# Kernel optimization log

Hardware: AMD Instinct MI355X
Metric: run time of the kernel (lower is better)

## Reference

```python
import jax, jax.numpy as jnp
import numpy as np

N_NODES = 20000
N_EDGES = 100000   # undirected input edges; make_directed doubles them
FEAT = 128
N_RBF = 20
NUM_CONV = 3
CUTOFF = 20.0
BOX = 10.0


def setup_inputs() -> dict:
    key = jax.random.key(0)
    ks = jax.random.split(key, 6)
    cg_xyz = jax.random.uniform(ks[0], (N_NODES, 3), jnp.float32) * BOX
    # random edges with no self-loops (avoid d=0 singularity in rbf/unit)
    src = jax.random.randint(ks[1], (N_EDGES,), 0, N_NODES)
    off = jax.random.randint(ks[2], (N_EDGES,), 1, N_NODES)
    CG_nbr_list = jnp.stack([src, (src + off) % N_NODES], axis=1)
    cg_s = jax.random.normal(ks[3], (N_NODES, FEAT), jnp.float32)

    def w(k, shape, fan_in):
        return (jax.random.normal(k, shape, jnp.float32) / np.float32(np.sqrt(fan_in)))
    kk = jax.random.split(ks[4], 7)
    params = dict(
        msg_W1=w(kk[0], (NUM_CONV, FEAT, FEAT), FEAT),
        msg_b1=jnp.zeros((NUM_CONV, FEAT), jnp.float32),
        msg_W2=w(kk[1], (NUM_CONV, 3 * FEAT, FEAT), FEAT),
        msg_b2=jnp.zeros((NUM_CONV, 3 * FEAT), jnp.float32),
        dist_W=w(kk[2], (NUM_CONV, 3 * FEAT, N_RBF), N_RBF),
        dist_b=jnp.zeros((NUM_CONV, 3 * FEAT), jnp.float32),
        upd_U=w(kk[3], (NUM_CONV, FEAT, FEAT), FEAT),
        upd_V=w(kk[4], (NUM_CONV, FEAT, FEAT), FEAT),
        upd_sW1=w(kk[5], (NUM_CONV, FEAT, 2 * FEAT), 2 * FEAT),
        upd_sb1=jnp.zeros((NUM_CONV, FEAT), jnp.float32),
        upd_sW2=w(kk[6], (NUM_CONV, 3 * FEAT, FEAT), FEAT),
        upd_sb2=jnp.zeros((NUM_CONV, 3 * FEAT), jnp.float32),
    )
    return dict(cg_xyz=cg_xyz, CG_nbr_list=CG_nbr_list, cg_s=cg_s, **params)


def _forward(cg_xyz, cg_s, nbr, msg_W1, msg_b1, msg_W2, msg_b2, dist_W, dist_b,
             upd_U, upd_V, upd_sW1, upd_sb1, upd_sW2, upd_sb2):
    N = cg_s.shape[0]
    # make_directed: input is undirected -> append flipped edges
    nbrs = jnp.concatenate([nbr, nbr[:, ::-1]], axis=0)   # [E, 2]
    i, j = nbrs[:, 0], nbrs[:, 1]
    r_ij = cg_xyz[j] - cg_xyz[i]                           # [E, 3]
    d = jnp.linalg.norm(r_ij, axis=-1)                     # [E]
    unit = r_ij / d[:, None]
    # PainnRadialBasis: sin(k*pi*d/cutoff)/d, k=1..n_rbf
    kvec = jnp.arange(1, N_RBF + 1, dtype=cg_xyz.dtype)
    rbf = jnp.sin(kvec * jnp.pi * d[:, None] / CUTOFF) / d[:, None]   # [E, n_rbf]
    # cosine envelope
    env = jnp.where(d < CUTOFF, 0.5 * (jnp.cos(jnp.pi * d / CUTOFF) + 1.0), 0.0)

    s = cg_s
    v = jnp.zeros((N, FEAT, 3), cg_s.dtype)
    for l in range(NUM_CONV):
        # ---- MessageBlock ----
        phi = jax.nn.silu(s @ msg_W1[l].T + msg_b1[l]) @ msg_W2[l].T + msg_b2[l]  # [N, 3F]
        w_s = (rbf @ dist_W[l].T + dist_b[l]) * env[:, None]                      # [E, 3F]
        inv = (phi[j] * w_s).reshape(-1, 3, FEAT)                                 # [E, 3, F]
        dv_ij = inv[:, 2, :, None] * unit[:, None, :] + inv[:, 0, :, None] * v[j] # [E, F, 3]
        s = s + jax.ops.segment_sum(inv[:, 1, :], i, num_segments=N)
        v = v + jax.ops.segment_sum(dv_ij, i, num_segments=N)
        # ---- UpdateBlock ----
        u_v = jnp.einsum('nfd,gf->ngd', v, upd_U[l])   # [N, F, 3]
        v_v = jnp.einsum('nfd,gf->ngd', v, upd_V[l])
        v_v_norm = jnp.linalg.norm(v_v, axis=-1)       # [N, F]
        a = (jax.nn.silu(jnp.concatenate([s, v_v_norm], -1) @ upd_sW1[l].T + upd_sb1[l])
             @ upd_sW2[l].T + upd_sb2[l]).reshape(-1, 3, FEAT)  # a_vv, a_sv, a_ss
        s = s + (u_v * v_v).sum(-1) * a[:, 1, :] + a[:, 2, :]
        v = v + u_v * a[:, 0, :, None]
    return s, v


def reference(cg_xyz, CG_nbr_list, cg_s, msg_W1, msg_b1, msg_W2, msg_b2, dist_W,
              dist_b, upd_U, upd_V, upd_sW1, upd_sb1, upd_sW2, upd_sb2):
    return _forward(cg_xyz, cg_s, CG_nbr_list, msg_W1, msg_b1, msg_W2, msg_b2,
                    dist_W, dist_b, upd_U, upd_V, upd_sW1, upd_sb1, upd_sW2, upd_sb2)
```

## Files before the change

### kernel.cpp

```cpp
#include <hip/hip_runtime.h>
#include <math.h>

#define FEAT 128
#define NRBF 20
#define NCONV 3
#define PI_F 3.14159265358979323846f

typedef __attribute__((ext_vector_type(8))) short short8;
typedef __attribute__((ext_vector_type(4))) float floatx4;
typedef unsigned short ushort_t;

__device__ inline float b2f(unsigned short u) {
    union { unsigned int i; float f; } c; c.i = ((unsigned int)u) << 16; return c.f;
}
__device__ inline unsigned short f2b(float x) {
    union { float f; unsigned int i; } c; c.f = x;
    unsigned int u = c.i;
    return (unsigned short)((u + 0x7fffu + ((u >> 16) & 1u)) >> 16);
}

template<int FUSED>
__global__ __launch_bounds__(256, 2) void mlp_fused_kernel(
    const float* __restrict__ s, const float* __restrict__ vv,
    const ushort_t* __restrict__ W1h, const ushort_t* __restrict__ W1l,
    const float* __restrict__ b1,
    const ushort_t* __restrict__ W2h, const ushort_t* __restrict__ W2l,
    const float* __restrict__ b2,
    ushort_t* __restrict__ out_b,
    const float* __restrict__ uv,
    float* s_out, float* vbuf,
    float* outv,
    int M, int K1, int SP)
{
    __shared__ __align__(16) ushort_t Ah[64 * 40];
    __shared__ __align__(16) ushort_t Al[64 * 40];
    __shared__ __align__(16) ushort_t Wh[128 * 40];
    __shared__ __align__(16) ushort_t Wl[128 * 40];
    __shared__ __align__(16) ushort_t Hh[64 * 136];
    __shared__ __align__(16) ushort_t Hl[64 * 136];

    const int t    = threadIdx.x;
    const int m0   = blockIdx.x * 64;
    const int wv   = t >> 6;
    const int lane = t & 63;
    const int wn   = wv * 32;
    const int lr   = lane & 15;
    const int lk   = (lane >> 4) * 8;
    const int quad = lane >> 4;
    const int arow = t >> 3;
    const int acol = (t & 7) * 4;
    const int wrow = t >> 2;
    const int wcol = (t & 3) * 8;

    floatx4 acc[4][2] = {};

    for (int k0 = 0; k0 < K1; k0 += 32) {
        #pragma unroll
        for (int h = 0; h < 2; ++h) {
            int r = arow + h * 32;
            int m = m0 + r; if (m >= M) m = M - 1;
            float xs[4];
            if (k0 < 128) {
                float4 av = *(const float4*)(s + (long)m * 128 + k0 + acol);
                xs[0] = av.x; xs[1] = av.y; xs[2] = av.z; xs[3] = av.w;
            } else {
                long base = (long)m * 128 + (k0 - 128 + acol);
                float4 a0 = *(const float4*)(vv + base);
                float4 a1 = *(const float4*)(vv + (long)SP + base);
                float4 a2 = *(const float4*)(vv + 2 * (long)SP + base);
                xs[0] = sqrtf(a0.x * a0.x + a1.x * a1.x + a2.x * a2.x);
                xs[1] = sqrtf(a0.y * a0.y + a1.y * a1.y + a2.y * a2.y);
                xs[2] = sqrtf(a0.z * a0.z + a1.z * a1.z + a2.z * a2.z);
                xs[3] = sqrtf(a0.w * a0.w + a1.w * a1.w + a2.w * a2.w);
            }
            unsigned short hh[4], ll[4];
            #pragma unroll
            for (int q = 0; q < 4; ++q) {
                hh[q] = f2b(xs[q]);
                ll[q] = f2b(xs[q] - b2f(hh[q]));
            }
            *(ushort4*)(&Ah[r * 40 + acol]) = make_ushort4(hh[0], hh[1], hh[2], hh[3]);
            *(ushort4*)(&Al[r * 40 + acol]) = make_ushort4(ll[0], ll[1], ll[2], ll[3]);
        }
        #pragma unroll
        for (int h = 0; h < 2; ++h) {
            int r = wrow + h * 64;
            *(uint4*)(&Wh[r * 40 + wcol]) =
                *(const uint4*)(W1h + (long)r * K1 + k0 + wcol);
            *(uint4*)(&Wl[r * 40 + wcol]) =
                *(const uint4*)(W1l + (long)r * K1 + k0 + wcol);
        }
        __syncthreads();
        short8 af[4], alf[4], wf[2], wlf[2];
        #pragma unroll
        for (int i = 0; i < 4; ++i) {
            af[i]  = *(const short8*)(&Ah[(i * 16 + lr) * 40 + lk]);
            alf[i] = *(const short8*)(&Al[(i * 16 + lr) * 40 + lk]);
        }
        #pragma unroll
        for (int j = 0; j < 2; ++j) {
            wf[j]  = *(const short8*)(&Wh[(wn + j * 16 + lr) * 40 + lk]);
            wlf[j] = *(const short8*)(&Wl[(wn + j * 16 + lr) * 40 + lk]);
        }
        #pragma unroll
        for (int i = 0; i < 4; ++i)
            #pragma unroll
            for (int j = 0; j < 2; ++j) {
                acc[i][j] = __builtin_amdgcn_mfma_f32_16x16x32_bf16(
                    af[i], wf[j], acc[i][j], 0, 0, 0);
                acc[i][j] = __builtin_amdgcn_mfma_f32_16x16x32_bf16(
                    af[i], wlf[j], acc[i][j], 0, 0, 0);
                acc[i][j] = __builtin_amdgcn_mfma_f32_16x16x32_bf16(
                    alf[i], wf[j], acc[i][j], 0, 0, 0);
            }
        __syncthreads();
    }

    #pragma unroll
    for (int i = 0; i < 4; ++i)
        #pragma unroll
        for (int r = 0; r < 4; ++r) {
            int mrow = i * 16 + quad * 4 + r;
            #pragma unroll
            for (int j = 0; j < 2; ++j) {
                int kcol = wn + j * 16 + lr;
                float x = acc[i][j][r] + b1[kcol];
                x *= 1.f / (1.f + __expf(-x));
                unsigned short hh = f2b(x);
                Hh[mrow * 136 + kcol] = hh;
                Hl[mrow * 136 + kcol] = f2b(x - b2f(hh));
            }
        }

    floatx4 accS[3][4][2];
    #pragma unroll
    for (int nt = 0; nt < 3; ++nt) {
        floatx4 a2c[4][2] = {};
        for (int k0 = 0; k0 < 128; k0 += 32) {
            __syncthreads();
            #pragma unroll
            for (int h = 0; h < 2; ++h) {
                int r = wrow + h * 64;
                long wo = (long)(nt * 128 + r) * 128;
                *(uint4*)(&Wh[r * 40 + wcol]) = *(const uint4*)(W2h + wo + k0 + wcol);
                *(uint4*)(&Wl[r * 40 + wcol]) = *(const uint4*)(W2l + wo + k0 + wcol);
            }
            __syncthreads();
            short8 af[4], alf[4], wf[2], wlf[2];
            #pragma unroll
            for (int i = 0; i < 4; ++i) {
                af[i]  = *(const short8*)(&Hh[(i * 16 + lr) * 136 + k0 + lk]);
                alf[i] = *(const short8*)(&Hl[(i * 16 + lr) * 136 + k0 + lk]);
            }
            #pragma unroll
            for (int j = 0; j < 2; ++j) {
                wf[j]  = *(const short8*)(&Wh[(wn + j * 16 + lr) * 40 + lk]);
                wlf[j] = *(const short8*)(&Wl[(wn + j * 16 + lr) * 40 + lk]);
            }
            #pragma unroll
            for (int i = 0; i < 4; ++i)
                #pragma unroll
                for (int j = 0; j < 2; ++j) {
                    a2c[i][j] = __builtin_amdgcn_mfma_f32_16x16x32_bf16(
                        af[i], wf[j], a2c[i][j], 0, 0, 0);
                    a2c[i][j] = __builtin_amdgcn_mfma_f32_16x16x32_bf16(
                        af[i], wlf[j], a2c[i][j], 0, 0, 0);
                    a2c[i][j] = __builtin_amdgcn_mfma_f32_16x16x32_bf16(
                        alf[i], wf[j], a2c[i][j], 0, 0, 0);
                }
        }
        if (FUSED) {
            #pragma unroll
            for (int i = 0; i < 4; ++i)
                #pragma unroll
                for (int j = 0; j < 2; ++j)
                    accS[nt][i][j] = a2c[i][j];
        } else {
            #pragma unroll
            for (int i = 0; i < 4; ++i)
                #pragma unroll
                for (int r = 0; r < 4; ++r) {
                    int m = m0 + i * 16 + quad * 4 + r;
                    if (m >= M) continue;
                    #pragma unroll
                    for (int j = 0; j < 2; ++j) {
                        int n = nt * 128 + wn + j * 16 + lr;
                        out_b[(long)m * 384 + n] = f2b(a2c[i][j][r] + b2[n]);
                    }
                }
        }
    }

    if (FUSED) {
        #pragma unroll
        for (int i = 0; i < 4; ++i)
            #pragma unroll
            for (int r = 0; r < 4; ++r) {
                int m = m0 + i * 16 + quad * 4 + r;
                if (m >= M) continue;
                #pragma unroll
                for (int j = 0; j < 2; ++j) {
                    int g = wn + j * 16 + lr;
                    long idx = (long)m * 128 + g;
                    float a0 = accS[0][i][j][r] + b2[g];
                    float a1 = accS[1][i][j][r] + b2[128 + g];
                    float a2 = accS[2][i][j][r] + b2[256 + g];
                    float u0 = uv[idx], u1 = uv[SP + idx], u2 = uv[2 * SP + idx];
                    float w0 = vv[idx], w1 = vv[SP + idx], w2 = vv[2 * SP + idx];
                    float dot = u0 * w0 + u1 * w1 + u2 * w2;
                    s_out[idx] = s[idx] + dot * a1 + a2;
                    float x0 = vbuf[idx]          + u0 * a0;
                    float x1 = vbuf[SP + idx]     + u1 * a0;
                    float x2 = vbuf[2 * SP + idx] + u2 * a0;
                    if (outv) {
                        outv[idx * 3 + 0] = x0;
                        outv[idx * 3 + 1] = x1;
                        outv[idx * 3 + 2] = x2;
                    } else {
                        vbuf[idx]          = x0;
                        vbuf[SP + idx]     = x1;
                        vbuf[2 * SP + idx] = x2;
                    }
                }
            }
    }
}

__global__ __launch_bounds__(256) void gemm_ps_kernel(
    const ushort_t* __restrict__ Ahg, const ushort_t* __restrict__ Alg,
    const ushort_t* __restrict__ Whi, const ushort_t* __restrict__ Wlo,
    const ushort_t* __restrict__ W2h, const ushort_t* __restrict__ W2l,
    float* __restrict__ C0, float* __restrict__ C1,
    int M, int K)
{
    __shared__ __align__(16) ushort_t Ah[128 * 40];
    __shared__ __align__(16) ushort_t Al[128 * 40];
    __shared__ __align__(16) ushort_t Wh[128 * 40];
    __shared__ __align__(16) ushort_t Wl[128 * 40];
    const int t    = threadIdx.x;
    const int m0   = blockIdx.x * 128;
    const int nt   = blockIdx.y;
    const int wv   = t >> 6;
    const int lane = t & 63;
    const int wm   = (wv >> 1) * 64;
    const int wn   = (wv & 1) * 64;
    const int lr   = lane & 15;
    const int lk   = (lane >> 4) * 8;
    const int srow = t >> 2;
    const int scol = (t & 3) * 8;
    const ushort_t* Wsh = nt ? W2h : Whi;
    const ushort_t* Wsl = nt ? W2l : Wlo;

    floatx4 acc[4][4] = {};

    for (int k0 = 0; k0 < K; k0 += 32) {
        #pragma unroll
        for (int h = 0; h < 2; ++h) {
            int r = srow + h * 64;
            int m = m0 + r; if (m >= M) m = M - 1;
            *(uint4*)(&Ah[r * 40 + scol]) =
                *(const uint4*)(Ahg + (long)m * K + k0 + scol);
            *(uint4*)(&Al[r * 40 + scol]) =
                *(const uint4*)(Alg + (long)m * K + k0 + scol);
            *(uint4*)(&Wh[r * 40 + scol]) =
                *(const uint4*)(Wsh + (long)r * K + k0 + scol);
            *(uint4*)(&Wl[r * 40 + scol]) =
                *(const uint4*)(Wsl + (long)r * K + k0 + scol);
        }
        __syncthreads();
        short8 ah[4], al[4], wh[4], wl[4];
        #pragma unroll
        for (int i = 0; i < 4; ++i) {
            ah[i] = *(const short8*)(&Ah[(wm + i * 16 + lr) * 40 + lk]);
            al[i] = *(const short8*)(&Al[(wm + i * 16 + lr) * 40 + lk]);
            wh[i] = *(const short8*)(&Wh[(wn + i * 16 + lr) * 40 + lk]);
            wl[i] = *(const short8*)(&Wl[(wn + i * 16 + lr) * 40 + lk]);
        }
        #pragma unroll
        for (int i = 0; i < 4; ++i)
            #pragma unroll
            for (int j = 0; j < 4; ++j) {
                acc[i][j] = __builtin_amdgcn_mfma_f32_16x16x32_bf16(
                    ah[i], wh[j], acc[i][j], 0, 0, 0);
                acc[i][j] = __builtin_amdgcn_mfma_f32_16x16x32_bf16(
                    ah[i], wl[j], acc[i][j], 0, 0, 0);
                acc[i][j] = __builtin_amdgcn_mfma_f32_16x16x32_bf16(
                    al[i], wh[j], acc[i][j], 0, 0, 0);
            }
        __syncthreads();
    }

    float* C = nt ? C1 : C0;
    #pragma unroll
    for (int i = 0; i < 4; ++i)
        #pragma unroll
        for (int r = 0; r < 4; ++r) {
            int m = m0 + wm + i * 16 + (lane >> 4) * 4 + r;
            if (m >= M) continue;
            #pragma unroll
            for (int j = 0; j < 4; ++j) {
                int n = wn + j * 16 + lr;
                C[(long)m * 128 + n] = acc[i][j][r];
            }
        }
}

__global__ __launch_bounds__(256) void split_kernel(
    const float* __restrict__ src, ushort_t* __restrict__ hi,
    ushort_t* __restrict__ lo, int n)
{
    int i = blockIdx.x * blockDim.x + threadIdx.x;
    if (i >= n) return;
    float x = src[i];
    unsigned short h = f2b(x);
    hi[i] = h;
    lo[i] = f2b(x - b2f(h));
}

__global__ __launch_bounds__(256) void hist_kernel(
    const int* __restrict__ nbr, int* __restrict__ deg, int Ed)
{
    int e = blockIdx.x * blockDim.x + threadIdx.x;
    if (e >= Ed) return;
    int E = Ed >> 1;
    int i = (e < E) ? nbr[2 * e] : nbr[2 * (e - E) + 1];
    atomicAdd(&deg[i], 1);
}

__device__ inline int wave_incl_scan(int x, int lane)
{
    #pragma unroll
    for (int s = 1; s < 64; s <<= 1) {
        int y = __shfl_up(x, s, 64);
        if (lane >= s) x += y;
    }
    return x;
}

__global__ __launch_bounds__(1024) void scan_kernel(
    const int* __restrict__ deg, int* __restrict__ off,
    int* __restrict__ cursor, int N)
{
    __shared__ int wsum[16];
    __shared__ int carry_s;
    const int t = threadIdx.x;
    const int lane = t & 63;
    const int w = t >> 6;
    if (t == 0) { carry_s = 0; off[0] = 0; }
    __syncthreads();
    for (int base = 0; base < N; base += 1024) {
        int i = base + t;
        int x = (i < N) ? deg[i] : 0;
        int sc = wave_incl_scan(x, lane);
        if (lane == 63) wsum[w] = sc;
        __syncthreads();
        if (w == 0) {
            int v = (lane < 16) ? wsum[lane] : 0;
            int vs = wave_incl_scan(v, lane);
            if (lane < 16) wsum[lane] = vs;
        }
        __syncthreads();
        int waveoff = (w > 0) ? wsum[w - 1] : 0;
        int inc = sc + waveoff + carry_s;
        if (i < N) { off[i + 1] = inc; cursor[i] = inc - x; }
        __syncthreads();
        if (t == 1023) carry_s = inc;
        __syncthreads();
    }
}

__global__ __launch_bounds__(256) void scatter_geom_kernel(
    const int* __restrict__ nbr, const float* __restrict__ xyz,
    int* __restrict__ cursor, int* __restrict__ csr_j,
    float* __restrict__ csr_env, float* __restrict__ csr_unit,
    float* __restrict__ csr_rbfe, int Ed)
{
    int e = blockIdx.x * blockDim.x + threadIdx.x;
    if (e >= Ed) return;
    int E = Ed >> 1;
    int i, j;
    if (e < E) { i = nbr[2 * e];         j = nbr[2 * e + 1]; }
    else       { int u = e - E; i = nbr[2 * u + 1]; j = nbr[2 * u]; }

    int p = atomicAdd(&cursor[i], 1);
    csr_j[p] = j;

    float rx = xyz[3 * j + 0] - xyz[3 * i + 0];
    float ry = xyz[3 * j + 1] - xyz[3 * i + 1];
    float rz = xyz[3 * j + 2] - xyz[3 * i + 2];
    float d   = sqrtf(rx * rx + ry * ry + rz * rz);
    float inv = 1.f / d;
    csr_unit[3 * p + 0] = rx * inv;
    csr_unit[3 * p + 1] = ry * inv;
    csr_unit[3 * p + 2] = rz * inv;
    float ev = (d < 20.f) ? 0.5f * (__cosf(PI_F * d / 20.f) + 1.f) : 0.f;
    csr_env[p] = ev;
    float base = PI_F * d / 20.f;
    #pragma unroll
    for (int k = 0; k < NRBF; ++k)
        csr_rbfe[(long)p * NRBF + k] = ev * __sinf((float)(k + 1) * base) * inv;
}

__global__ __launch_bounds__(128) void edge_aggr_kernel(
    const int* __restrict__ off, const int* __restrict__ csr_j,
    const float* __restrict__ csr_env, const float* __restrict__ csr_unit,
    const float* __restrict__ csr_rbfe,
    const ushort_t* __restrict__ phib, const float* __restrict__ vold,
    const float* __restrict__ distW, const float* __restrict__ distb,
    float* __restrict__ s, float* __restrict__ vnew,
    ushort_t* __restrict__ vnh, ushort_t* __restrict__ vnl, int N, int SP)
{
    const int f = threadIdx.x;
    float w0c[NRBF], w1c[NRBF], w2c[NRBF];
    const float b0 = distb[f];
    const float b1 = distb[128 + f];
    const float b2 = distb[256 + f];
    #pragma unroll
    for (int k = 0; k < NRBF; ++k) {
        w0c[k] = distW[(long)f * NRBF + k];
        w1c[k] = distW[(long)(128 + f) * NRBF + k];
        w2c[k] = distW[(long)(256 + f) * NRBF + k];
    }

    for (int node = blockIdx.x; node < N; node += gridDim.x) {
        const int p0 = off[node], p1 = off[node + 1];
        float ssum = 0.f, v0 = 0.f, v1 = 0.f, v2 = 0.f;
        for (int p = p0; p < p1; ++p) {
            int j = csr_j[p];
            float ev = csr_env[p];
            float ux = csr_unit[3 * p + 0];
            float uy = csr_unit[3 * p + 1];
            float uz = csr_unit[3 * p + 2];
            const float* rb = csr_rbfe + (long)p * NRBF;
            float w0 = ev * b0, w1 = ev * b1, w2 = ev * b2;
            #pragma unroll
            for (int k = 0; k < NRBF; ++k) {
                float r = rb[k];
                w0 += r * w0c[k];
                w1 += r * w1c[k];
                w2 += r * w2c[k];
            }
            long jb = (long)j * 384;
            float i0 = b2f(phib[jb + f])       * w0;
            float i1 = b2f(phib[jb + 128 + f]) * w1;
            float i2 = b2f(phib[jb + 256 + f]) * w2;
            long jv = (long)j * FEAT + f;
            ssum += i1;
            v0 += i2 * ux + i0 * vold[jv];
            v1 += i2 * uy + i0 * vold[SP + jv];
            v2 += i2 * uz + i0 * vold[2 * SP + jv];
        }
        long iv = (long)node * FEAT + f;
        s[iv] += ssum;
        float n0 = vold[iv]          + v0;
        float n1 = vold[SP + iv]     + v1;
        float n2 = vold[2 * SP + iv] + v2;
        vnew[iv]          = n0;
        vnew[SP + iv]     = n1;
        vnew[2 * SP + iv] = n2;
        unsigned short h0 = f2b(n0), h1 = f2b(n1), h2 = f2b(n2);
        vnh[iv]          = h0;  vnl[iv]          = f2b(n0 - b2f(h0));
        vnh[SP + iv]     = h1;  vnl[SP + iv]     = f2b(n1 - b2f(h1));
        vnh[2 * SP + iv] = h2;  vnl[2 * SP + iv] = f2b(n2 - b2f(h2));
    }
}

__global__ __launch_bounds__(256) void init_s_kernel(
    const float* __restrict__ cg_s, float* __restrict__ s,
    float* __restrict__ vA, int nS, int nV)
{
    int idx = blockIdx.x * blockDim.x + threadIdx.x;
    if (idx < nS) s[idx] = cg_s[idx];
    if (idx < nV) vA[idx] = 0.f;
}

extern "C" void kernel_launch(void* const* d_in, const int* in_sizes, int n_in,
                              void* d_out, int out_size, void* d_ws, size_t ws_size,
                              hipStream_t stream)
{
    const float* xyz     = (const float*)d_in[0];
    const int*   nbr     = (const int*)  d_in[1];
    const float* cg_s    = (const float*)d_in[2];
    const float* msg_W1  = (const float*)d_in[3];
    const float* msg_b1  = (const float*)d_in[4];
    const float* msg_W2  = (const float*)d_in[5];
    const float* msg_b2  = (const float*)d_in[6];
    const float* dist_W  = (const float*)d_in[7];
    const float* dist_b  = (const float*)d_in[8];
    const float* upd_U   = (const float*)d_in[9];
    const float* upd_V   = (const float*)d_in[10];
    const float* upd_sW1 = (const float*)d_in[11];
    const float* upd_sb1 = (const float*)d_in[12];
    const float* upd_sW2 = (const float*)d_in[13];
    const float* upd_sb2 = (const float*)d_in[14];

    const int E  = in_sizes[1] / 2;
    const int Ed = 2 * E;
    const int N  = in_sizes[2] / FEAT;
    const int SP = N * FEAT;

    float* s    = (float*)d_out;
    float* outv = (float*)d_out + (long)SP;

    float* w = (float*)d_ws;
    size_t off_ = 0;
    auto alloc = [&](size_t nelem) {
        float* p = w + off_;
        off_ += (nelem + 255) & ~(size_t)255;
        return p;
    };
    auto allocb = [&](size_t nelem) {
        return (ushort_t*)alloc((nelem + 1) / 2);
    };
    int*   deg      = (int*)alloc((size_t)N);
    int*   off      = (int*)alloc((size_t)N + 1);
    int*   cursor   = (int*)alloc((size_t)N);
    int*   csr_j    = (int*)alloc((size_t)Ed);
    float* csr_env  = alloc((size_t)Ed);
    float* csr_unit = alloc((size_t)Ed * 3);
    float* csr_rbfe = alloc((size_t)Ed * NRBF);
    float* u_v      = alloc((size_t)3 * SP);
    float* v_v      = alloc((size_t)3 * SP);
    float* vA       = alloc((size_t)3 * SP);
    float* vB       = alloc((size_t)3 * SP);
    ushort_t* phi_b = allocb((size_t)N * 384);
    ushort_t* vnh   = allocb((size_t)3 * SP);
    ushort_t* vnl   = allocb((size_t)3 * SP);
    const int n1 = NCONV * FEAT * FEAT;
    const int n2 = NCONV * 3 * FEAT * FEAT;
    const int n3 = NCONV * FEAT * 2 * FEAT;
    ushort_t* w1h  = allocb((size_t)n1);
    ushort_t* w1l  = allocb((size_t)n1);
    ushort_t* w2h  = allocb((size_t)n2);
    ushort_t* w2l  = allocb((size_t)n2);
    ushort_t* uh   = allocb((size_t)n1);
    ushort_t* ul   = allocb((size_t)n1);
    ushort_t* vh   = allocb((size_t)n1);
    ushort_t* vl   = allocb((size_t)n1);
    ushort_t* sw1h = allocb((size_t)n3);
    ushort_t* sw1l = allocb((size_t)n3);
    ushort_t* sw2h = allocb((size_t)n2);
    ushort_t* sw2l = allocb((size_t)n2);
    (void)ws_size; (void)n_in; (void)out_size;

    split_kernel<<<(n1 + 255) / 256, 256, 0, stream>>>(msg_W1, w1h, w1l, n1);
    split_kernel<<<(n2 + 255) / 256, 256, 0, stream>>>(msg_W2, w2h, w2l, n2);
    split_kernel<<<(n1 + 255) / 256, 256, 0, stream>>>(upd_U, uh, ul, n1);
    split_kernel<<<(n1 + 255) / 256, 256, 0, stream>>>(upd_V, vh, vl, n1);
    split_kernel<<<(n3 + 255) / 256, 256, 0, stream>>>(upd_sW1, sw1h, sw1l, n3);
    split_kernel<<<(n2 + 255) / 256, 256, 0, stream>>>(upd_sW2, sw2h, sw2l, n2);

    {
        int n = 3 * SP;
        init_s_kernel<<<(n + 255) / 256, 256, 0, stream>>>(cg_s, s, vA, SP, n);
    }

    hipMemsetAsync(deg, 0, (size_t)N * sizeof(int), stream);
    hist_kernel<<<(Ed + 255) / 256, 256, 0, stream>>>(nbr, deg, Ed);
    scan_kernel<<<1, 1024, 0, stream>>>(deg, off, cursor, N);
    scatter_geom_kernel<<<(Ed + 255) / 256, 256, 0, stream>>>(
        nbr, xyz, cursor, csr_j, csr_env, csr_unit, csr_rbfe, Ed);

    float* vold = vA;
    float* vnew = vB;
    dim3 gM((N + 63) / 64, 1);
    dim3 gUV((3 * N + 127) / 128, 2);
    int edgeGrid = 2048;
    if (edgeGrid > N) edgeGrid = N;

    for (int l = 0; l < NCONV; ++l) {
        const float* b1  = msg_b1  + (long)l * FEAT;
        const float* b2  = msg_b2  + (long)l * 3 * FEAT;
        const float* dW  = dist_W  + (long)l * 3 * FEAT * NRBF;
        const float* db  = dist_b  + (long)l * 3 * FEAT;
        const float* sb1 = upd_sb1 + (long)l * FEAT;
        const float* sb2 = upd_sb2 + (long)l * 3 * FEAT;
        const long o1 = (long)l * FEAT * FEAT;
        const long o2 = (long)l * 3 * FEAT * FEAT;
        const long o3 = (long)l * FEAT * 2 * FEAT;

        mlp_fused_kernel<0><<<gM, 256, 0, stream>>>(
            s, nullptr, w1h + o1, w1l + o1, b1, w2h + o2, w2l + o2, b2,
            phi_b, nullptr, nullptr, nullptr, nullptr, N, FEAT, SP);

        edge_aggr_kernel<<<edgeGrid, 128, 0, stream>>>(
            off, csr_j, csr_env, csr_unit, csr_rbfe, phi_b, vold,
            dW, db, s, vnew, vnh, vnl, N, SP);

        gemm_ps_kernel<<<gUV, 256, 0, stream>>>(
            vnh, vnl, uh + o1, ul + o1, vh + o1, vl + o1,
            u_v, v_v, 3 * N, FEAT);

        float* ov = (l == NCONV - 1) ? outv : nullptr;
        mlp_fused_kernel<1><<<gM, 256, 0, stream>>>(
            s, v_v, sw1h + o3, sw1l + o3, sb1, sw2h + o2, sw2l + o2, sb2,
            nullptr, u_v, s, vnew, ov, N, 2 * FEAT, SP);

        float* tmp = vold; vold = vnew; vnew = tmp;
    }
}
```

Before: 768.8 us.

## Fuse next layer's message MLP into update MLP kernel epilogue

Adds a MODE 2 variant of the MLP kernel that, after the update block, writes the new s tile into shared memory as a split bf16 hi/lo pair. It then runs the next layer's message MLP (W1, SiLU, W2) on that tile, so layers 1 and 2 no longer need a separate message MLP launch or a re-read of s from global memory. It also doubles the edge aggregation grid size. The trade is more shared-memory reuse, extra barriers and register pressure in the fused kernel against one fewer launch and less memory traffic per layer.

```diff
diff --git a/kernel.cpp b/kernel.cpp
--- a/kernel.cpp
+++ b/kernel.cpp
@@ -19,7 +19,7 @@
     return (unsigned short)((u + 0x7fffu + ((u >> 16) & 1u)) >> 16);
 }
 
-template<int FUSED>
+template<int MODE>
 __global__ __launch_bounds__(256, 2) void mlp_fused_kernel(
     const float* __restrict__ s, const float* __restrict__ vv,
     const ushort_t* __restrict__ W1h, const ushort_t* __restrict__ W1l,
@@ -30,6 +30,11 @@
     const float* __restrict__ uv,
     float* s_out, float* vbuf,
     float* outv,
+    const ushort_t* __restrict__ pW1h, const ushort_t* __restrict__ pW1l,
+    const float* __restrict__ pb1,
+    const ushort_t* __restrict__ pW2h, const ushort_t* __restrict__ pW2l,
+    const float* __restrict__ pb2,
+    ushort_t* __restrict__ pout,
     int M, int K1, int SP)
 {
     __shared__ __align__(16) ushort_t Ah[64 * 40];
@@ -169,7 +174,7 @@
                         alf[i], wf[j], a2c[i][j], 0, 0, 0);
                 }
         }
-        if (FUSED) {
+        if (MODE >= 1) {
             #pragma unroll
             for (int i = 0; i < 4; ++i)
                 #pragma unroll
@@ -191,7 +196,8 @@
         }
     }
 
-    if (FUSED) {
+    if (MODE >= 1) {
+        if (MODE == 2) __syncthreads();
         #pragma unroll
         for (int i = 0; i < 4; ++i)
             #pragma unroll
@@ -208,11 +214,18 @@
                     float u0 = uv[idx], u1 = uv[SP + idx], u2 = uv[2 * SP + idx];
                     float w0 = vv[idx], w1 = vv[SP + idx], w2 = vv[2 * SP + idx];
                     float dot = u0 * w0 + u1 * w1 + u2 * w2;
-                    s_out[idx] = s[idx] + dot * a1 + a2;
+                    float sn = s[idx] + dot * a1 + a2;
+                    s_out[idx] = sn;
+                    if (MODE == 2) {
+                        int mrow = i * 16 + quad * 4 + r;
+                        unsigned short sh = f2b(sn);
+                        Hh[mrow * 136 + g] = sh;
+                        Hl[mrow * 136 + g] = f2b(sn - b2f(sh));
+                    }
                     float x0 = vbuf[idx]          + u0 * a0;
                     float x1 = vbuf[SP + idx]     + u1 * a0;
                     float x2 = vbuf[2 * SP + idx] + u2 * a0;
-                    if (outv) {
+                    if (MODE == 1 && outv) {
                         outv[idx * 3 + 0] = x0;
                         outv[idx * 3 + 1] = x1;
                         outv[idx * 3 + 2] = x2;
@@ -223,6 +236,111 @@
                     }
                 }
             }
+    }
+
+    if (MODE == 2) {
+        __syncthreads();
+        floatx4 pacc[4][2] = {};
+        for (int k0 = 0; k0 < 128; k0 += 32) {
+            __syncthreads();
+            #pragma unroll
+            for (int h = 0; h < 2; ++h) {
+                int r = wrow + h * 64;
+                *(uint4*)(&Wh[r * 40 + wcol]) =
+                    *(const uint4*)(pW1h + (long)r * 128 + k0 + wcol);
+                *(uint4*)(&Wl[r * 40 + wcol]) =
+                    *(const uint4*)(pW1l + (long)r * 128 + k0 + wcol);
+            }
+            __syncthreads();
+            short8 af[4], alf[4], wf[2], wlf[2];
+            #pragma unroll
+            for (int i = 0; i < 4; ++i) {
+                af[i]  = *(const short8*)(&Hh[(i * 16 + lr) * 136 + k0 + lk]);
+                alf[i] = *(const short8*)(&Hl[(i * 16 + lr) * 136 + k0 + lk]);
+            }
+            #pragma unroll
+            for (int j = 0; j < 2; ++j) {
+                wf[j]  = *(const short8*)(&Wh[(wn + j * 16 + lr) * 40 + lk]);
+                wlf[j] = *(const short8*)(&Wl[(wn + j * 16 + lr) * 40 + lk]);
+            }
+            #pragma unroll
+            for (int i = 0; i < 4; ++i)
+                #pragma unroll
+                for (int j = 0; j < 2; ++j) {
+                    pacc[i][j] = __builtin_amdgcn_mfma_f32_16x16x32_bf16(
+                        af[i], wf[j], pacc[i][j], 0, 0, 0);
+                    pacc[i][j] = __builtin_amdgcn_mfma_f32_16x16x32_bf16(
+                        af[i], wlf[j], pacc[i][j], 0, 0, 0);
+                    pacc[i][j] = __builtin_amdgcn_mfma_f32_16x16x32_bf16(
+                        alf[i], wf[j], pacc[i][j], 0, 0, 0);
+                }
+        }
+        __syncthreads();
+        #pragma unroll
+        for (int i = 0; i < 4; ++i)
+            #pragma unroll
+            for (int r = 0; r < 4; ++r) {
+                int mrow = i * 16 + quad * 4 + r;
+                #pragma unroll
+                for (int j = 0; j < 2; ++j) {
+                    int kcol = wn + j * 16 + lr;
+                    float x = pacc[i][j][r] + pb1[kcol];
+                    x *= 1.f / (1.f + __expf(-x));
+                    unsigned short hh = f2b(x);
+                    Hh[mrow * 136 + kcol] = hh;
+                    Hl[mrow * 136 + kcol] = f2b(x - b2f(hh));
+                }
+            }
+        for (int nt = 0; nt < 3; ++nt) {
+            floatx4 c2[4][2] = {};
+            for (int k0 = 0; k0 < 128; k0 += 32) {
+                __syncthreads();
+                #pragma unroll
+                for (int h = 0; h < 2; ++h) {
+                    int r = wrow + h * 64;
+                    long wo = (long)(nt * 128 + r) * 128;
+                    *(uint4*)(&Wh[r * 40 + wcol]) =
+                        *(const uint4*)(pW2h + wo + k0 + wcol);
+                    *(uint4*)(&Wl[r * 40 + wcol]) =
+                        *(const uint4*)(pW2l + wo + k0 + wcol);
+                }
+                __syncthreads();
+                short8 af[4], alf[4], wf[2], wlf[2];
+                #pragma unroll
+                for (int i = 0; i < 4; ++i) {
+                    af[i]  = *(const short8*)(&Hh[(i * 16 + lr) * 136 + k0 + lk]);
+                    alf[i] = *(const short8*)(&Hl[(i * 16 + lr) * 136 + k0 + lk]);
+                }
+                #pragma unroll
+                for (int j = 0; j < 2; ++j) {
+                    wf[j]  = *(const short8*)(&Wh[(wn + j * 16 + lr) * 40 + lk]);
+                    wlf[j] = *(const short8*)(&Wl[(wn + j * 16 + lr) * 40 + lk]);
+                }
+                #pragma unroll
+                for (int i = 0; i < 4; ++i)
+                    #pragma unroll
+                    for (int j = 0; j < 2; ++j) {
+                        c2[i][j] = __builtin_amdgcn_mfma_f32_16x16x32_bf16(
+                            af[i], wf[j], c2[i][j], 0, 0, 0);
+                        c2[i][j] = __builtin_amdgcn_mfma_f32_16x16x32_bf16(
+                            af[i], wlf[j], c2[i][j], 0, 0, 0);
+                        c2[i][j] = __builtin_amdgcn_mfma_f32_16x16x32_bf16(
+                            alf[i], wf[j], c2[i][j], 0, 0, 0);
+                    }
+            }
+            #pragma unroll
+            for (int i = 0; i < 4; ++i)
+                #pragma unroll
+                for (int r = 0; r < 4; ++r) {
+                    int m = m0 + i * 16 + quad * 4 + r;
+                    if (m >= M) continue;
+                    #pragma unroll
+                    for (int j = 0; j < 2; ++j) {
+                        int n = nt * 128 + wn + j * 16 + lr;
+                        pout[(long)m * 384 + n] = f2b(c2[i][j][r] + pb2[n]);
+                    }
+                }
+        }
     }
 }
 
@@ -565,11 +683,10 @@
     float* vnew = vB;
     dim3 gM((N + 63) / 64, 1);
     dim3 gUV((3 * N + 127) / 128, 2);
-    int edgeGrid = 2048;
+    int edgeGrid = 4096;
     if (edgeGrid > N) edgeGrid = N;
 
     for (int l = 0; l < NCONV; ++l) {
-        const float* b1  = msg_b1  + (long)l * FEAT;
         const float* b2  = msg_b2  + (long)l * 3 * FEAT;
         const float* dW  = dist_W  + (long)l * 3 * FEAT * NRBF;
         const float* db  = dist_b  + (long)l * 3 * FEAT;
@@ -579,9 +696,14 @@
         const long o2 = (long)l * 3 * FEAT * FEAT;
         const long o3 = (long)l * FEAT * 2 * FEAT;
 
-        mlp_fused_kernel<0><<<gM, 256, 0, stream>>>(
-            s, nullptr, w1h + o1, w1l + o1, b1, w2h + o2, w2l + o2, b2,
-            phi_b, nullptr, nullptr, nullptr, nullptr, N, FEAT, SP);
+        if (l == 0) {
+            const float* b1 = msg_b1;
+            mlp_fused_kernel<0><<<gM, 256, 0, stream>>>(
+                s, nullptr, w1h, w1l, b1, w2h, w2l, b2,
+                phi_b, nullptr, nullptr, nullptr, nullptr,
+                nullptr, nullptr, nullptr, nullptr, nullptr, nullptr, nullptr,
+                N, FEAT, SP);
+        }
 
         edge_aggr_kernel<<<edgeGrid, 128, 0, stream>>>(
             off, csr_j, csr_env, csr_unit, csr_rbfe, phi_b, vold,
@@ -591,10 +713,23 @@
             vnh, vnl, uh + o1, ul + o1, vh + o1, vl + o1,
             u_v, v_v, 3 * N, FEAT);
 
-        float* ov = (l == NCONV - 1) ? outv : nullptr;
-        mlp_fused_kernel<1><<<gM, 256, 0, stream>>>(
-            s, v_v, sw1h + o3, sw1l + o3, sb1, sw2h + o2, sw2l + o2, sb2,
-            nullptr, u_v, s, vnew, ov, N, 2 * FEAT, SP);
+        if (l < NCONV - 1) {
+            const long o1n = (long)(l + 1) * FEAT * FEAT;
+            const long o2n = (long)(l + 1) * 3 * FEAT * FEAT;
+            const float* pb1 = msg_b1 + (long)(l + 1) * FEAT;
+            const float* pb2 = msg_b2 + (long)(l + 1) * 3 * FEAT;
+            mlp_fused_kernel<2><<<gM, 256, 0, stream>>>(
+                s, v_v, sw1h + o3, sw1l + o3, sb1, sw2h + o2, sw2l + o2, sb2,
+                nullptr, u_v, s, vnew, nullptr,
+                w1h + o1n, w1l + o1n, pb1, w2h + o2n, w2l + o2n, pb2, phi_b,
+                N, 2 * FEAT, SP);
+        } else {
+            mlp_fused_kernel<1><<<gM, 256, 0, stream>>>(
+                s, v_v, sw1h + o3, sw1l + o3, sb1, sw2h + o2, sw2l + o2, sb2,
+                nullptr, u_v, s, vnew, outv,
+                nullptr, nullptr, nullptr, nullptr, nullptr, nullptr, nullptr,
+                N, 2 * FEAT, SP);
+        }
 
         float* tmp = vold; vold = vnew; vnew = tmp;
     }
```

Measured after the change: 770.6 us. About the same (+0.2%).
